# Kernel tuning notes

Hardware: AMD Instinct MI355X
Metric: run time of the kernel (lower is better)

Reference implementation:

```python
import jax, jax.numpy as jnp
import numpy as np

N = 50000
E = 800000
G = 64  # number of graphs in each batch
IN_DIM = 128
HID = 64
NEG_SLOPE = 0.2


def _glorot(key, shape):
    fan = shape[0] + shape[-1] if len(shape) == 2 else int(np.prod(shape[1:])) + shape[-1]
    lim = float(np.sqrt(6.0 / fan))
    return jax.random.uniform(key, shape, jnp.float32, -lim, lim)


def setup_inputs() -> dict:
    key = jax.random.key(0)
    ks = jax.random.split(key, 16)
    x1 = jax.random.normal(ks[0], (N, IN_DIM), jnp.float32)
    x2 = jax.random.normal(ks[1], (N, IN_DIM), jnp.float32)
    edge_index1 = jax.random.randint(ks[2], (2, E), 0, N, jnp.int64)
    edge_index2 = jax.random.randint(ks[3], (2, E), 0, N, jnp.int64)
    batch1 = jnp.sort(jax.random.randint(ks[4], (N,), 0, G, jnp.int64))
    batch2 = jnp.sort(jax.random.randint(ks[5], (N,), 0, G, jnp.int64))
    # conv1: GATConv(IN_DIM, HID, heads=4)
    W1 = _glorot(ks[6], (IN_DIM, 4 * HID))
    a_src1 = _glorot(ks[7], (1, 4, HID))
    a_dst1 = _glorot(ks[8], (1, 4, HID))
    b1 = jnp.zeros((4 * HID,), jnp.float32)
    # conv2: GATConv(4*HID, HID, heads=1)
    W2 = _glorot(ks[9], (4 * HID, HID))
    a_src2 = _glorot(ks[10], (1, 1, HID))
    a_dst2 = _glorot(ks[11], (1, 1, HID))
    b2 = jnp.zeros((HID,), jnp.float32)
    return {"x1": x1, "edge_index1": edge_index1, "batch1": batch1,
            "x2": x2, "edge_index2": edge_index2, "batch2": batch2,
            "W1": W1, "a_src1": a_src1, "a_dst1": a_dst1, "b1": b1,
            "W2": W2, "a_src2": a_src2, "a_dst2": a_dst2, "b2": b2}


def gat_conv(x, src, dst, W, a_src, a_dst, b, n_nodes, heads, out_dim):
    """PyG GATConv with add_self_loops=True, negative_slope=0.2, concat=True."""
    h = (x @ W).reshape(n_nodes, heads, out_dim)            # [N,H,D]
    alpha_s = jnp.sum(h * a_src, axis=-1)                   # [N,H]
    alpha_d = jnp.sum(h * a_dst, axis=-1)                   # [N,H]
    e = alpha_s[src] + alpha_d[dst]                         # [E',H]
    e = jax.nn.leaky_relu(e, NEG_SLOPE)
    # segment softmax over incoming edges of each destination node
    e_max = jax.ops.segment_max(e, dst, num_segments=n_nodes)
    ex = jnp.exp(e - e_max[dst])
    denom = jax.ops.segment_sum(ex, dst, num_segments=n_nodes)
    alpha = ex / (denom[dst] + 1e-16)                       # [E',H]
    msg = h[src] * alpha[:, :, None]                        # [E',H,D]
    out = jax.ops.segment_sum(msg, dst, num_segments=n_nodes)
    return out.reshape(n_nodes, heads * out_dim) + b


def embed(x, edge_index, batch, W1, a_src1, a_dst1, b1, W2, a_src2, a_dst2, b2):
    loops = jnp.arange(N, dtype=edge_index.dtype)
    src = jnp.concatenate([edge_index[0], loops])
    dst = jnp.concatenate([edge_index[1], loops])
    h = jax.nn.elu(gat_conv(x, src, dst, W1, a_src1, a_dst1, b1, N, 4, HID))
    h = jax.nn.elu(gat_conv(h, src, dst, W2, a_src2, a_dst2, b2, N, 1, HID))
    # global_mean_pool over graph ids
    sums = jax.ops.segment_sum(h, batch, num_segments=G)
    cnt = jax.ops.segment_sum(jnp.ones((N,), h.dtype), batch, num_segments=G)
    return sums / jnp.maximum(cnt, 1.0)[:, None]


def reference(x1, edge_index1, batch1, x2, edge_index2, batch2,
              W1, a_src1, a_dst1, b1, W2, a_src2, a_dst2, b2):
    emb1 = embed(x1, edge_index1, batch1, W1, a_src1, a_dst1, b1, W2, a_src2, a_dst2, b2)
    emb2 = embed(x2, edge_index2, batch2, W1, a_src1, a_dst1, b1, W2, a_src2, a_dst2, b2)
    return (emb1, emb2)
```

## Files before the change

### kernel.cpp

```cpp
#include <hip/hip_runtime.h>
#include <cstdint>
#include <cstddef>

#define NNODES 50000
#define NEDGES 800000
#define NGR    64
#define INDIM  128
#define HIDD   64

typedef __attribute__((ext_vector_type(8))) short bf16x8;
typedef __attribute__((ext_vector_type(4))) float f32x4;

__device__ __forceinline__ float lrelu(float x) { return x > 0.f ? x : 0.2f * x; }
__device__ __forceinline__ float eluf(float x)  { return x > 0.f ? x : expm1f(x); }
__device__ __forceinline__ float bf2f(unsigned short u) {
    return __uint_as_float((unsigned int)u << 16);
}
__device__ __forceinline__ unsigned short f2bf(float x) {
    unsigned int u = __float_as_uint(x);
    return (unsigned short)((u + 0x7fffu + ((u >> 16) & 1u)) >> 16);
}

__global__ void cvt_f2b(const float* __restrict__ in, unsigned short* __restrict__ out, int n4) {
    int i = blockIdx.x * 256 + threadIdx.x;
    if (i < n4) {
        float4 v = ((const float4*)in)[i];
        ushort4 o;
        o.x = f2bf(v.x); o.y = f2bf(v.y); o.z = f2bf(v.z); o.w = f2bf(v.w);
        ((ushort4*)out)[i] = o;
    }
}

__global__ void count_dst(const int* __restrict__ ei0, const int* __restrict__ ei1,
                          int* __restrict__ cnt, int E, int N) {
    const int* ei = blockIdx.y ? ei1 : ei0;
    int* c = cnt + blockIdx.y * N;
    int e = blockIdx.x * 256 + threadIdx.x;
    if (e < E) atomicAdd(&c[ei[E + e]], 1);
}

__global__ __launch_bounds__(256) void scan_part(const int* __restrict__ cnt,
                                                 int* __restrict__ psum, int n) {
    __shared__ int ws[4];
    const int* c = cnt + blockIdx.y * n;
    int* p = psum + blockIdx.y * 256;
    int lane = threadIdx.x & 63, w = threadIdx.x >> 6;
    int i = blockIdx.x * 256 + threadIdx.x;
    int v = (i < n) ? c[i] : 0;
    #pragma unroll
    for (int off = 32; off >= 1; off >>= 1) v += __shfl_xor(v, off, 64);
    if (lane == 0) ws[w] = v;
    __syncthreads();
    if (threadIdx.x == 0) p[blockIdx.x] = ws[0] + ws[1] + ws[2] + ws[3];
}

__global__ __launch_bounds__(256) void scan_tops(int* __restrict__ psum,
                                                 int* __restrict__ rp, int nb, int n) {
    __shared__ int wsum[4];
    int* p = psum + blockIdx.x * 256;
    int* r = rp + blockIdx.x * (n + 1);
    int tid = threadIdx.x, lane = tid & 63, w = tid >> 6;
    int v = (tid < nb) ? p[tid] : 0;
    int x = v;
    #pragma unroll
    for (int off = 1; off < 64; off <<= 1) {
        int t = __shfl_up(x, off, 64);
        if (lane >= off) x += t;
    }
    if (lane == 63) wsum[w] = x;
    __syncthreads();
    int add = 0;
    for (int k = 0; k < w; k++) add += wsum[k];
    int incl = x + add;
    if (tid < nb) p[tid] = incl - v;
    if (tid == nb - 1) r[n] = incl;
}

__global__ __launch_bounds__(256) void scan_fin(const int* __restrict__ cnt,
                                                const int* __restrict__ psum,
                                                int* __restrict__ rp, int n) {
    __shared__ int wsum[4];
    const int* c = cnt + blockIdx.y * n;
    const int* p = psum + blockIdx.y * 256;
    int* r = rp + blockIdx.y * (n + 1);
    int tid = threadIdx.x, lane = tid & 63, w = tid >> 6;
    int i = blockIdx.x * 256 + tid;
    int v = (i < n) ? c[i] : 0;
    int x = v;
    #pragma unroll
    for (int off = 1; off < 64; off <<= 1) {
        int t = __shfl_up(x, off, 64);
        if (lane >= off) x += t;
    }
    if (lane == 63) wsum[w] = x;
    __syncthreads();
    int add = p[blockIdx.x];
    for (int k = 0; k < w; k++) add += wsum[k];
    if (i < n) r[i] = x + add - v;
}

__global__ void fill_csr(const int* __restrict__ ei0, const int* __restrict__ ei1,
                         const int* __restrict__ rp, int* __restrict__ fc,
                         int* __restrict__ col, int E, int N) {
    int g = blockIdx.y;
    const int* ei = g ? ei1 : ei0;
    const int* r = rp + g * (N + 1);
    int* f = fc + g * N;
    int* cl = col + (size_t)g * E;
    int e = blockIdx.x * 256 + threadIdx.x;
    if (e < E) {
        int s = ei[e];
        int d = ei[E + e];
        int pos = atomicAdd(&f[d], 1);
        cl[r[d] + pos] = s;
    }
}

template<int BN, int WM, int WN, bool AF32>
__global__ __launch_bounds__(256) void gemm_mfma(const void* __restrict__ A0,
                                                 const void* __restrict__ A1,
                                                 size_t Ags,
                                                 const unsigned short* __restrict__ Bw,
                                                 unsigned short* __restrict__ C,
                                                 size_t Cgs,
                                                 int M, int K, int N,
                                                 const float* __restrict__ a_src,
                                                 const float* __restrict__ a_dst,
                                                 float* __restrict__ as_o,
                                                 float* __restrict__ ad_o,
                                                 int hstride, int ags) {
    constexpr int BM = 128, BK = 64;
    constexpr int MI = WM / 16, NI = WN / 16;
    constexpr int LDA = BK + 8;
    __shared__ unsigned short Asm[BM * LDA];
    __shared__ unsigned short Bsm[BN * LDA];
    int gph = blockIdx.z;
    const float* Af = (const float*)(gph ? A1 : A0);
    const unsigned short* Ab = (const unsigned short*)A0 + (size_t)gph * Ags;
    unsigned short* Cg = C + (size_t)gph * Cgs;
    float* aso = as_o + (size_t)gph * ags;
    float* ado = ad_o + (size_t)gph * ags;
    int tid = threadIdx.x;
    int lane = tid & 63, wave = tid >> 6;
    int l15 = lane & 15, quad = lane >> 4;
    int wm0, wn0;
    if (BN == 128) { wm0 = (wave >> 1) * 64; wn0 = (wave & 1) * 64; }
    else           { wm0 = wave * 32;        wn0 = 0; }
    int row0 = blockIdx.x * BM;
    int c0 = blockIdx.y * BN;

    f32x4 acc[MI][NI];
    #pragma unroll
    for (int mi = 0; mi < MI; mi++)
        #pragma unroll
        for (int ni = 0; ni < NI; ni++)
            acc[mi][ni] = (f32x4){0.f, 0.f, 0.f, 0.f};

    for (int k0 = 0; k0 < K; k0 += BK) {
        #pragma unroll
        for (int q = 0; q < BM / 32; q++) {
            int idx = q * 256 + tid;
            int r = idx >> 3, kc = idx & 7;
            int row = row0 + r;
            if (AF32) {
                float4 v0 = make_float4(0.f, 0.f, 0.f, 0.f), v1 = v0;
                if (row < M) {
                    v0 = *(const float4*)(Af + (size_t)row * K + k0 + kc * 8);
                    v1 = *(const float4*)(Af + (size_t)row * K + k0 + kc * 8 + 4);
                }
                unsigned short t[8] = {f2bf(v0.x), f2bf(v0.y), f2bf(v0.z), f2bf(v0.w),
                                       f2bf(v1.x), f2bf(v1.y), f2bf(v1.z), f2bf(v1.w)};
                *(uint4*)&Asm[r * LDA + kc * 8] = *(uint4*)t;
            } else {
                uint4 v = make_uint4(0u, 0u, 0u, 0u);
                if (row < M) v = *(const uint4*)(Ab + (size_t)row * K + k0 + kc * 8);
                *(uint4*)&Asm[r * LDA + kc * 8] = v;
            }
        }
        #pragma unroll
        for (int q = 0; q < BN / 32; q++) {
            int idx = q * 256 + tid;
            int n  = idx & (BN - 1);
            int kc = idx / BN;
            unsigned short tmp[8];
            #pragma unroll
            for (int j = 0; j < 8; j++)
                tmp[j] = Bw[(size_t)(k0 + kc * 8 + j) * N + c0 + n];
            *(uint4*)&Bsm[n * LDA + kc * 8] = *(uint4*)tmp;
        }
        __syncthreads();
        #pragma unroll
        for (int kb = 0; kb < 2; kb++) {
            bf16x8 af[MI], bfr[NI];
            #pragma unroll
            for (int mi = 0; mi < MI; mi++)
                af[mi] = *(bf16x8*)&Asm[(wm0 + mi * 16 + l15) * LDA + kb * 32 + quad * 8];
            #pragma unroll
            for (int ni = 0; ni < NI; ni++)
                bfr[ni] = *(bf16x8*)&Bsm[(wn0 + ni * 16 + l15) * LDA + kb * 32 + quad * 8];
            #pragma unroll
            for (int mi = 0; mi < MI; mi++)
                #pragma unroll
                for (int ni = 0; ni < NI; ni++)
                    acc[mi][ni] = __builtin_amdgcn_mfma_f32_16x16x32_bf16(
                        af[mi], bfr[ni], acc[mi][ni], 0, 0, 0);
        }
        __syncthreads();
    }
    #pragma unroll
    for (int mi = 0; mi < MI; mi++) {
        #pragma unroll
        for (int r = 0; r < 4; r++) {
            int row = row0 + wm0 + mi * 16 + quad * 4 + r;
            if (row < M) {
                #pragma unroll
                for (int ni = 0; ni < NI; ni++) {
                    int colg = c0 + wn0 + ni * 16 + l15;
                    Cg[(size_t)row * N + colg] = f2bf(acc[mi][ni][r]);
                }
            }
        }
    }
    int headc = (c0 + wn0) >> 6;
    float a_s[NI], a_d[NI];
    #pragma unroll
    for (int ni = 0; ni < NI; ni++) {
        a_s[ni] = a_src[headc * 64 + ni * 16 + l15];
        a_d[ni] = a_dst[headc * 64 + ni * 16 + l15];
    }
    #pragma unroll
    for (int mi = 0; mi < MI; mi++) {
        #pragma unroll
        for (int r = 0; r < 4; r++) {
            float ps = 0.f, pd = 0.f;
            #pragma unroll
            for (int ni = 0; ni < NI; ni++) {
                ps += acc[mi][ni][r] * a_s[ni];
                pd += acc[mi][ni][r] * a_d[ni];
            }
            #pragma unroll
            for (int off = 1; off < 16; off <<= 1) {
                ps += __shfl_xor(ps, off, 64);
                pd += __shfl_xor(pd, off, 64);
            }
            int row = row0 + wm0 + mi * 16 + quad * 4 + r;
            if (l15 == 0 && row < M) {
                aso[row * hstride + headc] = ps;
                ado[row * hstride + headc] = pd;
            }
        }
    }
}

__global__ __launch_bounds__(256) void agg_h4(const unsigned short* __restrict__ h,
                                              size_t hgs,
                                              const float* __restrict__ as_,
                                              const float* __restrict__ ad_, int ags,
                                              const int* __restrict__ rp,
                                              const int* __restrict__ col,
                                              const float* __restrict__ bias,
                                              unsigned short* __restrict__ out,
                                              size_t ogs, int n, int E) {
    int gph = blockIdx.y;
    const uint2* h2v = (const uint2*)(h + (size_t)gph * hgs);
    const float* as = as_ + (size_t)gph * ags;
    const float* adp = ad_ + (size_t)gph * ags;
    const int* r = rp + gph * (n + 1);
    const int* cl = col + (size_t)gph * E;
    unsigned short* og = out + (size_t)gph * ogs;

    int wave = threadIdx.x >> 6, lane = threadIdx.x & 63;
    int node = blockIdx.x * 4 + wave;
    if (node >= n) return;
    int head = lane >> 4, l15 = lane & 15, q16 = lane & 48;
    float adv = adp[node * 4 + head];
    float w0 = __expf(lrelu(as[node * 4 + head] + adv));
    uint2 hu = h2v[(size_t)node * 64 + lane];
    float den = w0;
    float ax = __uint_as_float(hu.x << 16) * w0;
    float ay = __uint_as_float(hu.x & 0xffff0000u) * w0;
    float az = __uint_as_float(hu.y << 16) * w0;
    float aw = __uint_as_float(hu.y & 0xffff0000u) * w0;
    int beg = __builtin_amdgcn_readfirstlane(r[node]);
    int end = __builtin_amdgcn_readfirstlane(r[node + 1]);
    for (int j = beg; j < end; j += 16) {
        int m = end - j; if (m > 16) m = 16;
        int colv = cl[j + (l15 < m ? l15 : m - 1)];
        float av = as[colv * 4 + head];
        float w = __expf(lrelu(av + adv));
        int e = 0;
        for (; e + 2 <= m; e += 2) {
            float wa = __shfl(w, q16 | e);
            float wb = __shfl(w, q16 | (e + 1));
            int s0 = __shfl(colv, e);
            int s1 = __shfl(colv, e + 1);
            uint2 u0 = h2v[(size_t)s0 * 64 + lane];
            uint2 u1 = h2v[(size_t)s1 * 64 + lane];
            den += wa + wb;
            ax += __uint_as_float(u0.x << 16) * wa + __uint_as_float(u1.x << 16) * wb;
            ay += __uint_as_float(u0.x & 0xffff0000u) * wa + __uint_as_float(u1.x & 0xffff0000u) * wb;
            az += __uint_as_float(u0.y << 16) * wa + __uint_as_float(u1.y << 16) * wb;
            aw += __uint_as_float(u0.y & 0xffff0000u) * wa + __uint_as_float(u1.y & 0xffff0000u) * wb;
        }
        if (e < m) {
            float wa = __shfl(w, q16 | e);
            int s0 = __shfl(colv, e);
            uint2 u0 = h2v[(size_t)s0 * 64 + lane];
            den += wa;
            ax += __uint_as_float(u0.x << 16) * wa;
            ay += __uint_as_float(u0.x & 0xffff0000u) * wa;
            az += __uint_as_float(u0.y << 16) * wa;
            aw += __uint_as_float(u0.y & 0xffff0000u) * wa;
        }
    }
    float rden = 1.f / (den + 1e-16f);
    float4 bv = ((const float4*)bias)[lane];
    ushort4 o;
    o.x = f2bf(eluf(ax * rden + bv.x));
    o.y = f2bf(eluf(ay * rden + bv.y));
    o.z = f2bf(eluf(az * rden + bv.z));
    o.w = f2bf(eluf(aw * rden + bv.w));
    ((ushort4*)og)[(size_t)node * 64 + lane] = o;
}

__global__ __launch_bounds__(256) void agg_h1(const unsigned short* __restrict__ h,
                                              size_t hgs,
                                              const float* __restrict__ as_,
                                              const float* __restrict__ ad_,
                                              const int* __restrict__ rp,
                                              const int* __restrict__ col,
                                              const float* __restrict__ bias,
                                              float* __restrict__ out,
                                              size_t ogs, int n, int E) {
    int gph = blockIdx.y;
    const unsigned short* hg = h + (size_t)gph * hgs;
    const float* as = as_ + (size_t)gph * n;
    const float* adp = ad_ + (size_t)gph * n;
    const int* r = rp + gph * (n + 1);
    const int* cl = col + (size_t)gph * E;
    float* og = out + (size_t)gph * ogs;

    int wave = threadIdx.x >> 6, lane = threadIdx.x & 63;
    int node = blockIdx.x * 4 + wave;
    if (node >= n) return;
    float adv = adp[node];
    float w0 = __expf(lrelu(as[node] + adv));
    float den = w0;
    float acc = w0 * bf2f(hg[(size_t)node * 64 + lane]);
    int beg = __builtin_amdgcn_readfirstlane(r[node]);
    int end = __builtin_amdgcn_readfirstlane(r[node + 1]);
    for (int j = beg; j < end; j += 64) {
        int m = end - j; if (m > 64) m = 64;
        int colv = cl[j + (lane < m ? lane : m - 1)];
        float w = __expf(lrelu(as[colv] + adv));
        int e = 0;
        for (; e + 2 <= m; e += 2) {
            float wa = __shfl(w, e);
            float wb = __shfl(w, e + 1);
            int s0 = __shfl(colv, e);
            int s1 = __shfl(colv, e + 1);
            float va = bf2f(hg[(size_t)s0 * 64 + lane]);
            float vb = bf2f(hg[(size_t)s1 * 64 + lane]);
            den += wa + wb;
            acc += va * wa + vb * wb;
        }
        if (e < m) {
            float wa = __shfl(w, e);
            int s0 = __shfl(colv, e);
            den += wa;
            acc += wa * bf2f(hg[(size_t)s0 * 64 + lane]);
        }
    }
    float rden = 1.f / (den + 1e-16f);
    og[(size_t)node * 64 + lane] = eluf(acc * rden + bias[lane]);
}

__device__ __forceinline__ int lbound(const int* __restrict__ a, int n, int key) {
    int lo = 0, hi = n;
    while (lo < hi) {
        int mid = (lo + hi) >> 1;
        if (a[mid] < key) lo = mid + 1; else hi = mid;
    }
    return lo;
}

__global__ __launch_bounds__(256) void pool_mean(const float* __restrict__ g2,
                                                 size_t ggs,
                                                 const int* __restrict__ b0,
                                                 const int* __restrict__ b1,
                                                 float* __restrict__ out, int n) {
    __shared__ float red[4][64];
    __shared__ int bnds[2];
    int gph = blockIdx.y;
    const int* batch = gph ? b1 : b0;
    const float* gg = g2 + (size_t)gph * ggs;
    float* og = out + (size_t)gph * NGR * HIDD;
    int g = blockIdx.x;
    if (threadIdx.x < 2) bnds[threadIdx.x] = lbound(batch, n, g + (int)threadIdx.x);
    __syncthreads();
    int s = bnds[0], e = bnds[1];
    int lane = threadIdx.x & 63, wave = threadIdx.x >> 6;
    float acc = 0.f;
    for (int i = s + wave; i < e; i += 4)
        acc += gg[(size_t)i * 64 + lane];
    red[wave][lane] = acc;
    __syncthreads();
    if (wave == 0) {
        float sum = red[0][lane] + red[1][lane] + red[2][lane] + red[3][lane];
        og[g * 64 + lane] = sum / fmaxf((float)(e - s), 1.0f);
    }
}

extern "C" void kernel_launch(void* const* d_in, const int* in_sizes, int n_in,
                              void* d_out, int out_size, void* d_ws, size_t ws_size,
                              hipStream_t stream) {
    const int N = NNODES, E = NEDGES;

    const float* x1 = (const float*)d_in[0];
    const float* x2 = (const float*)d_in[3];
    const int* ei1v = (const int*)d_in[1];
    const int* ei2v = (const int*)d_in[4];
    const int* ba1  = (const int*)d_in[2];
    const int* ba2  = (const int*)d_in[5];
    const float* W1     = (const float*)d_in[6];
    const float* a_src1 = (const float*)d_in[7];
    const float* a_dst1 = (const float*)d_in[8];
    const float* b1     = (const float*)d_in[9];
    const float* W2     = (const float*)d_in[10];
    const float* a_src2 = (const float*)d_in[11];
    const float* a_dst2 = (const float*)d_in[12];
    const float* b2     = (const float*)d_in[13];

    char* ws = (char*)d_ws;
    size_t off = 0;
    auto carve = [&](size_t bytes) -> char* {
        char* p = ws + off;
        off = (off + bytes + 255) & ~(size_t)255;
        return p;
    };
    char* R1 = carve((size_t)2 * N * 256 * 2);
    char* R2 = carve((size_t)2 * N * 256 * 2);
    char* R3 = carve((size_t)2 * N * 64 * 2);
    int*   col  = (int*)carve((size_t)2 * E * 4);
    int*   rp   = (int*)carve((size_t)2 * (N + 1) * 4);
    int*   cntN = (int*)carve((size_t)2 * N * 4);
    int*   psum = (int*)carve(2 * 256 * 4);
    float* as1  = (float*)carve((size_t)2 * N * 4 * 4);
    float* ad1  = (float*)carve((size_t)2 * N * 4 * 4);
    float* as2  = (float*)carve((size_t)2 * N * 4);
    float* ad2  = (float*)carve((size_t)2 * N * 4);
    unsigned short* W1b = (unsigned short*)carve(INDIM * 256 * 2);
    unsigned short* W2b = (unsigned short*)carve(256 * HIDD * 2);

    unsigned short* h1 = (unsigned short*)R1;
    unsigned short* g1 = (unsigned short*)R2;
    unsigned short* h2 = (unsigned short*)R3;
    float* g2 = (float*)R1;

    float* outF = (float*)d_out;

    const int nodeBlocks = (N + 3) / 4;
    const int nb = (N + 255) / 256;
    const int eb = (E + 255) / 256;

    cvt_f2b<<<(INDIM * 256 / 4 + 255) / 256, 256, 0, stream>>>(W1, W1b, INDIM * 256 / 4);
    cvt_f2b<<<(256 * HIDD / 4 + 255) / 256, 256, 0, stream>>>(W2, W2b, 256 * HIDD / 4);

    hipMemsetAsync(cntN, 0, (size_t)2 * N * 4, stream);
    count_dst<<<dim3(eb, 2), 256, 0, stream>>>(ei1v, ei2v, cntN, E, N);
    scan_part<<<dim3(nb, 2), 256, 0, stream>>>(cntN, psum, N);
    scan_tops<<<2, 256, 0, stream>>>(psum, rp, nb, N);
    scan_fin<<<dim3(nb, 2), 256, 0, stream>>>(cntN, psum, rp, N);
    hipMemsetAsync(cntN, 0, (size_t)2 * N * 4, stream);
    fill_csr<<<dim3(eb, 2), 256, 0, stream>>>(ei1v, ei2v, rp, cntN, col, E, N);

    gemm_mfma<128, 64, 64, true><<<dim3(391, 2, 2), 256, 0, stream>>>(
        x1, x2, 0, W1b, h1, (size_t)N * 256, N, INDIM, 256,
        a_src1, a_dst1, as1, ad1, 4, N * 4);
    agg_h4<<<dim3(nodeBlocks, 2), 256, 0, stream>>>(h1, (size_t)N * 256, as1, ad1, N * 4,
                                                    rp, col, b1, g1, (size_t)N * 256, N, E);

    gemm_mfma<64, 32, 64, false><<<dim3(391, 1, 2), 256, 0, stream>>>(
        g1, nullptr, (size_t)N * 256, W2b, h2, (size_t)N * 64, N, 256, HIDD,
        a_src2, a_dst2, as2, ad2, 1, N);
    agg_h1<<<dim3(nodeBlocks, 2), 256, 0, stream>>>(h2, (size_t)N * 64, as2, ad2,
                                                    rp, col, b2, g2, (size_t)N * 64, N, E);

    pool_mean<<<dim3(NGR, 2), 256, 0, stream>>>(g2, (size_t)N * 64, ba1, ba2, outF, N);
}
```

Baseline: 572.9 us.

## Gather neighbor features with 16-byte loads, splitting edges across lane groups

Both aggregation kernels now gather each neighbor row with 16-byte uint4 loads per lane. In the 4-head layer-1 kernel, the wave splits into two halves that each take alternate edges. In the 1-head layer-2 kernel, the wave splits into eight groups of eight lanes that each take every eighth edge. The partial sums are then combined with xor-shuffle reductions, and only the first group writes the output. The aim is fewer, wider memory transactions and more edges in flight per wave. The cost is extra shuffle reductions, more accumulator registers, and masked-out work when a node's degree is not a multiple of the group count.

```diff
diff --git a/kernel.cpp b/kernel.cpp
--- a/kernel.cpp
+++ b/kernel.cpp
@@ -20,6 +20,8 @@
     unsigned int u = __float_as_uint(x);
     return (unsigned short)((u + 0x7fffu + ((u >> 16) & 1u)) >> 16);
 }
+__device__ __forceinline__ float lo16(unsigned int u) { return __uint_as_float(u << 16); }
+__device__ __forceinline__ float hi16(unsigned int u) { return __uint_as_float(u & 0xffff0000u); }
 
 __global__ void cvt_f2b(const float* __restrict__ in, unsigned short* __restrict__ out, int n4) {
     int i = blockIdx.x * 256 + threadIdx.x;
@@ -262,7 +264,7 @@
                                               unsigned short* __restrict__ out,
                                               size_t ogs, int n, int E) {
     int gph = blockIdx.y;
-    const uint2* h2v = (const uint2*)(h + (size_t)gph * hgs);
+    const uint4* h4 = (const uint4*)(h + (size_t)gph * hgs);
     const float* as = as_ + (size_t)gph * ags;
     const float* adp = ad_ + (size_t)gph * ags;
     const int* r = rp + gph * (n + 1);
@@ -272,55 +274,56 @@
     int wave = threadIdx.x >> 6, lane = threadIdx.x & 63;
     int node = blockIdx.x * 4 + wave;
     if (node >= n) return;
-    int head = lane >> 4, l15 = lane & 15, q16 = lane & 48;
-    float adv = adp[node * 4 + head];
-    float w0 = __expf(lrelu(as[node * 4 + head] + adv));
-    uint2 hu = h2v[(size_t)node * 64 + lane];
-    float den = w0;
-    float ax = __uint_as_float(hu.x << 16) * w0;
-    float ay = __uint_as_float(hu.x & 0xffff0000u) * w0;
-    float az = __uint_as_float(hu.y << 16) * w0;
-    float aw = __uint_as_float(hu.y & 0xffff0000u) * w0;
+    int p = lane >> 5;
+    int c = lane & 31;
+    int headc = c >> 3;
+    int l15 = lane & 15, quad = lane >> 4;
+    float adv_q = adp[node * 4 + quad];
+    float w0 = __expf(lrelu(as[node * 4 + headc] + adp[node * 4 + headc]));
+    float m0 = (p == 0) ? w0 : 0.f;
+    uint4 hu = h4[(size_t)node * 32 + c];
+    float den = m0;
+    float a0 = lo16(hu.x) * m0, a1 = hi16(hu.x) * m0;
+    float a2 = lo16(hu.y) * m0, a3 = hi16(hu.y) * m0;
+    float a4 = lo16(hu.z) * m0, a5 = hi16(hu.z) * m0;
+    float a6 = lo16(hu.w) * m0, a7 = hi16(hu.w) * m0;
     int beg = __builtin_amdgcn_readfirstlane(r[node]);
     int end = __builtin_amdgcn_readfirstlane(r[node + 1]);
+    int hbase = headc << 4;
     for (int j = beg; j < end; j += 16) {
         int m = end - j; if (m > 16) m = 16;
         int colv = cl[j + (l15 < m ? l15 : m - 1)];
-        float av = as[colv * 4 + head];
-        float w = __expf(lrelu(av + adv));
-        int e = 0;
-        for (; e + 2 <= m; e += 2) {
-            float wa = __shfl(w, q16 | e);
-            float wb = __shfl(w, q16 | (e + 1));
-            int s0 = __shfl(colv, e);
-            int s1 = __shfl(colv, e + 1);
-            uint2 u0 = h2v[(size_t)s0 * 64 + lane];
-            uint2 u1 = h2v[(size_t)s1 * 64 + lane];
-            den += wa + wb;
-            ax += __uint_as_float(u0.x << 16) * wa + __uint_as_float(u1.x << 16) * wb;
-            ay += __uint_as_float(u0.x & 0xffff0000u) * wa + __uint_as_float(u1.x & 0xffff0000u) * wb;
-            az += __uint_as_float(u0.y << 16) * wa + __uint_as_float(u1.y << 16) * wb;
-            aw += __uint_as_float(u0.y & 0xffff0000u) * wa + __uint_as_float(u1.y & 0xffff0000u) * wb;
-        }
-        if (e < m) {
-            float wa = __shfl(w, q16 | e);
-            int s0 = __shfl(colv, e);
-            uint2 u0 = h2v[(size_t)s0 * 64 + lane];
-            den += wa;
-            ax += __uint_as_float(u0.x << 16) * wa;
-            ay += __uint_as_float(u0.x & 0xffff0000u) * wa;
-            az += __uint_as_float(u0.y << 16) * wa;
-            aw += __uint_as_float(u0.y & 0xffff0000u) * wa;
-        }
-    }
-    float rden = 1.f / (den + 1e-16f);
-    float4 bv = ((const float4*)bias)[lane];
-    ushort4 o;
-    o.x = f2bf(eluf(ax * rden + bv.x));
-    o.y = f2bf(eluf(ay * rden + bv.y));
-    o.z = f2bf(eluf(az * rden + bv.z));
-    o.w = f2bf(eluf(aw * rden + bv.w));
-    ((ushort4*)og)[(size_t)node * 64 + lane] = o;
+        float wl = __expf(lrelu(as[colv * 4 + quad] + adv_q));
+        for (int base = 0; base < m; base += 2) {
+            int e = base + p;
+            int ec = e < m ? e : m - 1;
+            float we = __shfl(wl, hbase | ec);
+            if (e >= m) we = 0.f;
+            int s = __shfl(colv, ec);
+            uint4 u = h4[(size_t)s * 32 + c];
+            den += we;
+            a0 += lo16(u.x) * we; a1 += hi16(u.x) * we;
+            a2 += lo16(u.y) * we; a3 += hi16(u.y) * we;
+            a4 += lo16(u.z) * we; a5 += hi16(u.z) * we;
+            a6 += lo16(u.w) * we; a7 += hi16(u.w) * we;
+        }
+    }
+    den += __shfl_xor(den, 32);
+    a0 += __shfl_xor(a0, 32); a1 += __shfl_xor(a1, 32);
+    a2 += __shfl_xor(a2, 32); a3 += __shfl_xor(a3, 32);
+    a4 += __shfl_xor(a4, 32); a5 += __shfl_xor(a5, 32);
+    a6 += __shfl_xor(a6, 32); a7 += __shfl_xor(a7, 32);
+    if (p == 0) {
+        float rden = 1.f / (den + 1e-16f);
+        float4 b0 = ((const float4*)bias)[c * 2];
+        float4 b1 = ((const float4*)bias)[c * 2 + 1];
+        unsigned short t[8];
+        t[0] = f2bf(eluf(a0 * rden + b0.x)); t[1] = f2bf(eluf(a1 * rden + b0.y));
+        t[2] = f2bf(eluf(a2 * rden + b0.z)); t[3] = f2bf(eluf(a3 * rden + b0.w));
+        t[4] = f2bf(eluf(a4 * rden + b1.x)); t[5] = f2bf(eluf(a5 * rden + b1.y));
+        t[6] = f2bf(eluf(a6 * rden + b1.z)); t[7] = f2bf(eluf(a7 * rden + b1.w));
+        ((uint4*)(og + (size_t)node * 256))[c] = *(uint4*)t;
+    }
 }
 
 __global__ __launch_bounds__(256) void agg_h1(const unsigned short* __restrict__ h,
@@ -333,7 +336,7 @@
                                               float* __restrict__ out,
                                               size_t ogs, int n, int E) {
     int gph = blockIdx.y;
-    const unsigned short* hg = h + (size_t)gph * hgs;
+    const uint4* h4 = (const uint4*)(h + (size_t)gph * hgs);
     const float* as = as_ + (size_t)gph * n;
     const float* adp = ad_ + (size_t)gph * n;
     const int* r = rp + gph * (n + 1);
@@ -343,36 +346,58 @@
     int wave = threadIdx.x >> 6, lane = threadIdx.x & 63;
     int node = blockIdx.x * 4 + wave;
     if (node >= n) return;
+    int p = lane >> 3;
+    int c = lane & 7;
     float adv = adp[node];
     float w0 = __expf(lrelu(as[node] + adv));
-    float den = w0;
-    float acc = w0 * bf2f(hg[(size_t)node * 64 + lane]);
+    float m0 = (p == 0) ? w0 : 0.f;
+    uint4 hu = h4[(size_t)node * 8 + c];
+    float den = m0;
+    float a0 = lo16(hu.x) * m0, a1 = hi16(hu.x) * m0;
+    float a2 = lo16(hu.y) * m0, a3 = hi16(hu.y) * m0;
+    float a4 = lo16(hu.z) * m0, a5 = hi16(hu.z) * m0;
+    float a6 = lo16(hu.w) * m0, a7 = hi16(hu.w) * m0;
     int beg = __builtin_amdgcn_readfirstlane(r[node]);
     int end = __builtin_amdgcn_readfirstlane(r[node + 1]);
     for (int j = beg; j < end; j += 64) {
         int m = end - j; if (m > 64) m = 64;
         int colv = cl[j + (lane < m ? lane : m - 1)];
-        float w = __expf(lrelu(as[colv] + adv));
-        int e = 0;
-        for (; e + 2 <= m; e += 2) {
-            float wa = __shfl(w, e);
-            float wb = __shfl(w, e + 1);
-            int s0 = __shfl(colv, e);
-            int s1 = __shfl(colv, e + 1);
-            float va = bf2f(hg[(size_t)s0 * 64 + lane]);
-            float vb = bf2f(hg[(size_t)s1 * 64 + lane]);
-            den += wa + wb;
-            acc += va * wa + vb * wb;
-        }
-        if (e < m) {
-            float wa = __shfl(w, e);
-            int s0 = __shfl(colv, e);
-            den += wa;
-            acc += wa * bf2f(hg[(size_t)s0 * 64 + lane]);
-        }
-    }
-    float rden = 1.f / (den + 1e-16f);
-    og[(size_t)node * 64 + lane] = eluf(acc * rden + bias[lane]);
+        float wl = __expf(lrelu(as[colv] + adv));
+        for (int base = 0; base < m; base += 8) {
+            int e = base + p;
+            int ec = e < m ? e : m - 1;
+            float we = __shfl(wl, ec);
+            if (e >= m) we = 0.f;
+            int s = __shfl(colv, ec);
+            uint4 u = h4[(size_t)s * 8 + c];
+            den += we;
+            a0 += lo16(u.x) * we; a1 += hi16(u.x) * we;
+            a2 += lo16(u.y) * we; a3 += hi16(u.y) * we;
+            a4 += lo16(u.z) * we; a5 += hi16(u.z) * we;
+            a6 += lo16(u.w) * we; a7 += hi16(u.w) * we;
+        }
+    }
+    #pragma unroll
+    for (int off = 8; off < 64; off <<= 1) {
+        den += __shfl_xor(den, off);
+        a0 += __shfl_xor(a0, off); a1 += __shfl_xor(a1, off);
+        a2 += __shfl_xor(a2, off); a3 += __shfl_xor(a3, off);
+        a4 += __shfl_xor(a4, off); a5 += __shfl_xor(a5, off);
+        a6 += __shfl_xor(a6, off); a7 += __shfl_xor(a7, off);
+    }
+    if (p == 0) {
+        float rden = 1.f / (den + 1e-16f);
+        float4 b0 = ((const float4*)bias)[c * 2];
+        float4 b1 = ((const float4*)bias)[c * 2 + 1];
+        float4 o0, o1;
+        o0.x = eluf(a0 * rden + b0.x); o0.y = eluf(a1 * rden + b0.y);
+        o0.z = eluf(a2 * rden + b0.z); o0.w = eluf(a3 * rden + b0.w);
+        o1.x = eluf(a4 * rden + b1.x); o1.y = eluf(a5 * rden + b1.y);
+        o1.z = eluf(a6 * rden + b1.z); o1.w = eluf(a7 * rden + b1.w);
+        float* orow = og + (size_t)node * 64 + c * 8;
+        *(float4*)orow = o0;
+        *(float4*)(orow + 4) = o1;
+    }
 }
 
 __device__ __forceinline__ int lbound(const int* __restrict__ a, int n, int key) {
```

After: 559.5 us. 1.02x faster.
